# Kernel optimization log

Measured on AMD Instinct MI355X. Metric: run time of the kernel, lower is better.

The kernel has to match this reference:

```python
import jax, jax.numpy as jnp
import numpy as np

N_NODES = 50000
N_EDGES = 800000


def _gat_conv(x, src, dst, n, W, a_src, a_dst, b, concat):
    # x: [N, Fin]; W: [Fin, H*C]; a_src/a_dst: [H, C]; b: [H*C] or [C]
    H, C = a_src.shape
    h = (x @ W).reshape(n, H, C)                     # [N,H,C]
    alpha_src = jnp.sum(h * a_src[None], axis=-1)    # [N,H]
    alpha_dst = jnp.sum(h * a_dst[None], axis=-1)    # [N,H]
    e = alpha_src[src] + alpha_dst[dst]              # [E,H]
    e = jax.nn.leaky_relu(e, negative_slope=0.2)
    # segment softmax over incoming edges of each dst node
    m = jax.ops.segment_max(e, dst, num_segments=n)  # [N,H]
    ex = jnp.exp(e - m[dst])
    s = jax.ops.segment_sum(ex, dst, num_segments=n)
    alpha = ex / (s[dst] + 1e-16)                    # [E,H]
    msg = h[src] * alpha[:, :, None]                 # [E,H,C]
    out = jax.ops.segment_sum(msg, dst, num_segments=n)  # [N,H,C]
    out = out.reshape(n, H * C) if concat else out.mean(axis=1)
    return out + b


def setup_inputs() -> dict:
    key = jax.random.key(0)
    ks = jax.random.split(key, 12)
    d = {}
    d['x'] = jax.random.normal(ks[0], (N_NODES, 128), dtype=jnp.float32)
    d['edge_index'] = jax.random.randint(ks[1], (2, N_EDGES), 0, N_NODES, dtype=jnp.int32)
    s = 0.1
    d['w1'] = jax.random.normal(ks[2], (128, 128), dtype=jnp.float32) * s
    d['att_src1'] = jax.random.normal(ks[3], (2, 64), dtype=jnp.float32) * s
    d['att_dst1'] = jax.random.normal(ks[4], (2, 64), dtype=jnp.float32) * s
    d['b1'] = jnp.zeros((128,), jnp.float32)
    d['w2'] = jax.random.normal(ks[5], (128, 128), dtype=jnp.float32) * s
    d['att_src2'] = jax.random.normal(ks[6], (2, 64), dtype=jnp.float32) * s
    d['att_dst2'] = jax.random.normal(ks[7], (2, 64), dtype=jnp.float32) * s
    d['b2'] = jnp.zeros((128,), jnp.float32)
    d['w3'] = jax.random.normal(ks[8], (128, 40), dtype=jnp.float32) * s
    d['att_src3'] = jax.random.normal(ks[9], (1, 40), dtype=jnp.float32) * s
    d['att_dst3'] = jax.random.normal(ks[10], (1, 40), dtype=jnp.float32) * s
    d['b3'] = jnp.zeros((40,), jnp.float32)
    return d


def reference(x, edge_index, w1, att_src1, att_dst1, b1,
              w2, att_src2, att_dst2, b2, w3, att_src3, att_dst3, b3):
    n = x.shape[0]
    # PyG GATConv adds self-loops by default
    loop = jnp.arange(n, dtype=edge_index.dtype)
    src = jnp.concatenate([edge_index[0], loop])
    dst = jnp.concatenate([edge_index[1], loop])
    h = _gat_conv(x, src, dst, n, w1, att_src1, att_dst1, b1, concat=True)
    h = jax.nn.elu(h)  # dropout skipped (eval mode)
    h = _gat_conv(h, src, dst, n, w2, att_src2, att_dst2, b2, concat=True)
    h = jax.nn.elu(h)
    out = _gat_conv(h, src, dst, n, w3, att_src3, att_dst3, b3, concat=False)
    return out
```

## Files before the change

kernel.cpp:

```cpp
#include <hip/hip_runtime.h>
#include <hip/hip_fp16.h>

#define NN 50000
#define NE 800000
#define E2 850000
#define SCAN_NB 49
#define GEMM_BLKS 782
#define RANK_BLKS 3321

static inline int cdiv(long long a, int b) { return (int)((a + b - 1) / b); }

using half8  = __attribute__((ext_vector_type(8))) _Float16;
using floatx4 = __attribute__((ext_vector_type(4))) float;

struct __align__(16) h2x4 { __half2 a, b, c, d; };
struct __align__(8)  h2x2 { __half2 a, b; };

__device__ __forceinline__ void edge_sd(const int* __restrict__ ei, int e, int& s, int& d) {
    if (e < NE) { s = ei[e]; d = ei[NE + e]; }
    else { s = e - NE; d = s; }
}

__global__ __launch_bounds__(256) void prep_rank(const int* __restrict__ ei,
                                                 int* __restrict__ deg,
                                                 int* __restrict__ rank,
                                                 const float* __restrict__ x, __half* __restrict__ x16,
                                                 const float* __restrict__ w1, __half* __restrict__ wt1,
                                                 const float* __restrict__ w2, __half* __restrict__ wt2,
                                                 const float* __restrict__ w3, __half* __restrict__ wt3) {
    int b = blockIdx.x;
    if (b < RANK_BLKS) {
        int e = b * 256 + threadIdx.x;
        if (e < E2) {
            int d = (e < NE) ? ei[NE + e] : (e - NE);
            rank[e] = atomicAdd(&deg[d], 1);
        }
        return;
    }
    int tid = (b - RANK_BLKS) * 256 + threadIdx.x;
    int stride = (gridDim.x - RANK_BLKS) * 256;
    for (int i = tid; i < NN * 32; i += stride) {
        float4 v = *(const float4*)&x[(size_t)i * 4];
        h2x2 st;
        st.a = __floats2half2_rn(v.x, v.y);
        st.b = __floats2half2_rn(v.z, v.w);
        *(h2x2*)&x16[(size_t)i * 4] = st;
    }
    for (int i = tid; i < 128 * 128; i += stride)
        wt1[i] = __float2half(w1[(i & 127) * 128 + (i >> 7)]);
    for (int i = tid; i < 128 * 128; i += stride)
        wt2[i] = __float2half(w2[(i & 127) * 128 + (i >> 7)]);
    for (int i = tid; i < 40 * 128; i += stride)
        wt3[i] = __float2half(w3[(i & 127) * 40 + (i >> 7)]);
}

__global__ __launch_bounds__(256) void scan_all(const int* __restrict__ deg,
                                                int* __restrict__ rowp,
                                                int* __restrict__ bsums,
                                                int* __restrict__ ctr) {
    __shared__ int wsum[4];
    __shared__ int sh_pref[64];
    int tid = threadIdx.x;
    int base = blockIdx.x * 1024 + tid * 4;
    int4 v = make_int4(0, 0, 0, 0);
    if (base + 3 < NN) v = *(const int4*)&deg[base];
    else {
        if (base + 0 < NN) v.x = deg[base + 0];
        if (base + 1 < NN) v.y = deg[base + 1];
        if (base + 2 < NN) v.z = deg[base + 2];
    }
    v.y += v.x; v.z += v.y; v.w += v.z;
    int lane = tid & 63;
    int wid = tid >> 6;
    int t = v.w;
#pragma unroll
    for (int off = 1; off < 64; off <<= 1) {
        int u = __shfl_up(t, off, 64);
        if (lane >= off) t += u;
    }
    int excl = t - v.w;
    if (lane == 63) wsum[wid] = t;
    __syncthreads();
    int woff = 0;
    for (int w = 0; w < wid; ++w) woff += wsum[w];
    int add = excl + woff;
    if (tid == 255) {
        bsums[blockIdx.x] = add + v.w;
        __threadfence();
        atomicAdd(ctr, 1);
    }
    if (tid == 0) {
        while (__hip_atomic_load(ctr, __ATOMIC_ACQUIRE, __HIP_MEMORY_SCOPE_AGENT) < SCAN_NB) {
            __builtin_amdgcn_s_sleep(8);
        }
    }
    __syncthreads();
    if (tid < 64) {
        int bv = (tid < SCAN_NB)
            ? __hip_atomic_load(&bsums[tid], __ATOMIC_RELAXED, __HIP_MEMORY_SCOPE_AGENT) : 0;
        int s = bv;
#pragma unroll
        for (int off = 1; off < 64; off <<= 1) {
            int u = __shfl_up(s, off, 64);
            if (tid >= off) s += u;
        }
        sh_pref[tid] = s - bv;
    }
    __syncthreads();
    int boff = sh_pref[blockIdx.x];
    if (base == 0) rowp[0] = 0;
    if (base + 0 < NN) rowp[base + 1] = v.x + add + boff;
    if (base + 1 < NN) rowp[base + 2] = v.y + add + boff;
    if (base + 2 < NN) rowp[base + 3] = v.z + add + boff;
    if (base + 3 < NN) rowp[base + 4] = v.w + add + boff;
}

template<int MOUT, int H>
__device__ __forceinline__ void gemm_body(int bid, const __half* __restrict__ X,
                                          const __half* __restrict__ WT,
                                          const float* __restrict__ aS,
                                          const float* __restrict__ aD,
                                          __half* __restrict__ Ho,
                                          float* __restrict__ osrc,
                                          float* __restrict__ odst,
                                          __half* wlds) {
    constexpr int NT = (MOUT + 15) / 16;
    constexpr int NR = NT * 16;
    const int tid = threadIdx.x;
    for (int i = tid * 8; i < MOUT * 128; i += 2048) {
        half8 v = *(const half8*)&WT[i];
        *(half8*)&wlds[(i >> 7) * 136 + (i & 127)] = v;
    }
    if (NR > MOUT) {
        for (int i = tid * 8; i < (NR - MOUT) * 128; i += 2048) {
            half8 z = {};
            *(half8*)&wlds[(MOUT + (i >> 7)) * 136 + (i & 127)] = z;
        }
    }
    __syncthreads();

    const int lane = tid & 63;
    const int wid = tid >> 6;
    const int r0 = bid * 64 + wid * 16;
    const int arow = r0 + (lane & 15);
    const int lrow = (arow < NN) ? arow : (NN - 1);
    const int koff = (lane >> 4) * 8;
    const size_t xbase = (size_t)lrow * 128 + koff;
    half8 a0 = *(const half8*)&X[xbase];
    half8 a1 = *(const half8*)&X[xbase + 32];
    half8 a2 = *(const half8*)&X[xbase + 64];
    half8 a3 = *(const half8*)&X[xbase + 96];

    floatx4 acc[NT];
#pragma unroll
    for (int t = 0; t < NT; ++t) acc[t] = (floatx4){0.f, 0.f, 0.f, 0.f};

#pragma unroll
    for (int t = 0; t < NT; ++t) {
        const __half* wp = &wlds[(t * 16 + (lane & 15)) * 136 + koff];
        half8 b0 = *(const half8*)&wp[0];
        half8 b1 = *(const half8*)&wp[32];
        half8 b2 = *(const half8*)&wp[64];
        half8 b3 = *(const half8*)&wp[96];
        acc[t] = __builtin_amdgcn_mfma_f32_16x16x32_f16(a0, b0, acc[t], 0, 0, 0);
        acc[t] = __builtin_amdgcn_mfma_f32_16x16x32_f16(a1, b1, acc[t], 0, 0, 0);
        acc[t] = __builtin_amdgcn_mfma_f32_16x16x32_f16(a2, b2, acc[t], 0, 0, 0);
        acc[t] = __builtin_amdgcn_mfma_f32_16x16x32_f16(a3, b3, acc[t], 0, 0, 0);
    }

    const int cc = lane & 15;
    const int rbase = r0 + (lane >> 4) * 4;
    float ps[H][4], pd[H][4];
#pragma unroll
    for (int h = 0; h < H; ++h)
#pragma unroll
        for (int r = 0; r < 4; ++r) { ps[h][r] = 0.f; pd[h][r] = 0.f; }

#pragma unroll
    for (int t = 0; t < NT; ++t) {
        const int col = t * 16 + cc;
        const bool cv = (col < MOUT);
        const float as_ = cv ? aS[col] : 0.f;
        const float ad_ = cv ? aD[col] : 0.f;
        const int h = (H == 2) ? (t >> 2) : 0;
#pragma unroll
        for (int r = 0; r < 4; ++r) {
            ps[h][r] = fmaf(acc[t][r], as_, ps[h][r]);
            pd[h][r] = fmaf(acc[t][r], ad_, pd[h][r]);
        }
    }

    if constexpr (MOUT == 128) {
        __syncthreads();
        const int rowbase = wid * 16;
#pragma unroll
        for (int t = 0; t < NT; ++t)
#pragma unroll
            for (int r = 0; r < 4; ++r)
                wlds[(rowbase + (lane >> 4) * 4 + r) * 136 + t * 16 + cc] =
                    __float2half(acc[t][r]);
        __syncthreads();
#pragma unroll
        for (int p2 = 0; p2 < 4; ++p2) {
            int f = (p2 * 64 + lane) * 8;
            int row = f >> 7, col = f & 127;
            h2x4 v = *(h2x4*)&wlds[(rowbase + row) * 136 + col];
            int grow = r0 + row;
            if (grow < NN) *(h2x4*)&Ho[(size_t)grow * 128 + col] = v;
        }
    } else {
#pragma unroll
        for (int t = 0; t < NT; ++t) {
            const int col = t * 16 + cc;
            const bool cv = (col < MOUT);
#pragma unroll
            for (int r = 0; r < 4; ++r) {
                const int m = rbase + r;
                if (cv && m < NN) Ho[(size_t)m * MOUT + col] = __float2half(acc[t][r]);
            }
        }
    }

#pragma unroll
    for (int off = 1; off <= 8; off <<= 1) {
#pragma unroll
        for (int h = 0; h < H; ++h)
#pragma unroll
            for (int r = 0; r < 4; ++r) {
                ps[h][r] += __shfl_xor(ps[h][r], off, 64);
                pd[h][r] += __shfl_xor(pd[h][r], off, 64);
            }
    }
    if (cc == 0) {
#pragma unroll
        for (int r = 0; r < 4; ++r) {
            const int m = rbase + r;
            if (m < NN) {
#pragma unroll
                for (int h = 0; h < H; ++h) {
                    osrc[m * H + h] = ps[h][r];
                    odst[m * H + h] = pd[h][r];
                }
            }
        }
    }
}

__global__ __launch_bounds__(256) void gemm16_k128(const __half* __restrict__ X,
                                                   const __half* __restrict__ WT,
                                                   const float* __restrict__ aS,
                                                   const float* __restrict__ aD,
                                                   __half* __restrict__ Ho,
                                                   float* __restrict__ osrc,
                                                   float* __restrict__ odst) {
    __shared__ __half wlds[128 * 136];
    gemm_body<128, 2>(blockIdx.x, X, WT, aS, aD, Ho, osrc, odst, wlds);
}

__global__ __launch_bounds__(256) void gemm16_k40(const __half* __restrict__ X,
                                                  const __half* __restrict__ WT,
                                                  const float* __restrict__ aS,
                                                  const float* __restrict__ aD,
                                                  __half* __restrict__ Ho,
                                                  float* __restrict__ osrc,
                                                  float* __restrict__ odst) {
    __shared__ __half wlds[48 * 136];
    gemm_body<40, 1>(blockIdx.x, X, WT, aS, aD, Ho, osrc, odst, wlds);
}

__global__ __launch_bounds__(256) void gemm1_scat(const __half* __restrict__ X,
                                                  const __half* __restrict__ WT,
                                                  const float* __restrict__ aS,
                                                  const float* __restrict__ aD,
                                                  __half* __restrict__ Ho,
                                                  float* __restrict__ osrc,
                                                  float* __restrict__ odst,
                                                  const int* __restrict__ ei,
                                                  const int* __restrict__ rowp,
                                                  const int* __restrict__ rank,
                                                  int* __restrict__ csr_src) {
    __shared__ __half wlds[128 * 136];
    if (blockIdx.x < GEMM_BLKS) {
        gemm_body<128, 2>(blockIdx.x, X, WT, aS, aD, Ho, osrc, odst, wlds);
        return;
    }
    int e = (blockIdx.x - GEMM_BLKS) * 256 + threadIdx.x;
    if (e >= E2) return;
    int s, d; edge_sd(ei, e, s, d);
    csr_src[rowp[d] + rank[e]] = s;
}

__global__ __launch_bounds__(256) void agg_h2(const int* __restrict__ rowp,
                                              const int* __restrict__ csr_src,
                                              const __half* __restrict__ Hf,
                                              const float* __restrict__ osrc,
                                              const float* __restrict__ odst,
                                              const float* __restrict__ bias,
                                              __half* __restrict__ outp) {
    int n = blockIdx.x * 4 + (threadIdx.x >> 6);
    if (n >= NN) return;
    int lane = threadIdx.x & 63;
    int i0 = rowp[n], i1 = rowp[n + 1];
    int c = lane & 15;
    int slot = lane >> 4;
    int c8 = c * 8;
    int h2 = c >> 3;
    float adh = odst[n * 2 + h2];
    bool pl = ((c & 7) == 0);

    float4 lo0{0.f,0.f,0.f,0.f}, hi0{0.f,0.f,0.f,0.f};
    float4 lo1{0.f,0.f,0.f,0.f}, hi1{0.f,0.f,0.f,0.f};
    float psum = 0.f;

    int idx = i0 + slot;
    for (; idx + 12 < i1; idx += 16) {
        int s0 = csr_src[idx];
        int s1 = csr_src[idx + 4];
        int s2 = csr_src[idx + 8];
        int s3 = csr_src[idx + 12];
        float e0 = osrc[s0 * 2 + h2] + adh;
        float e1 = osrc[s1 * 2 + h2] + adh;
        float e2 = osrc[s2 * 2 + h2] + adh;
        float e3 = osrc[s3 * 2 + h2] + adh;
        e0 = (e0 >= 0.f) ? e0 : 0.2f * e0;
        e1 = (e1 >= 0.f) ? e1 : 0.2f * e1;
        e2 = (e2 >= 0.f) ? e2 : 0.2f * e2;
        e3 = (e3 >= 0.f) ? e3 : 0.2f * e3;
        float p0 = __expf(e0), p1 = __expf(e1), p2 = __expf(e2), p3 = __expf(e3);
        h2x4 hv0 = *(const h2x4*)&Hf[(size_t)s0 * 128 + c8];
        h2x4 hv1 = *(const h2x4*)&Hf[(size_t)s1 * 128 + c8];
        h2x4 hv2 = *(const h2x4*)&Hf[(size_t)s2 * 128 + c8];
        h2x4 hv3 = *(const h2x4*)&Hf[(size_t)s3 * 128 + c8];
        if (pl) psum += (p0 + p1) + (p2 + p3);
        float2 f;
        f = __half22float2(hv0.a); lo0.x = fmaf(f.x, p0, lo0.x); lo0.y = fmaf(f.y, p0, lo0.y);
        f = __half22float2(hv0.b); lo0.z = fmaf(f.x, p0, lo0.z); lo0.w = fmaf(f.y, p0, lo0.w);
        f = __half22float2(hv0.c); hi0.x = fmaf(f.x, p0, hi0.x); hi0.y = fmaf(f.y, p0, hi0.y);
        f = __half22float2(hv0.d); hi0.z = fmaf(f.x, p0, hi0.z); hi0.w = fmaf(f.y, p0, hi0.w);
        f = __half22float2(hv1.a); lo0.x = fmaf(f.x, p1, lo0.x); lo0.y = fmaf(f.y, p1, lo0.y);
        f = __half22float2(hv1.b); lo0.z = fmaf(f.x, p1, lo0.z); lo0.w = fmaf(f.y, p1, lo0.w);
        f = __half22float2(hv1.c); hi0.x = fmaf(f.x, p1, hi0.x); hi0.y = fmaf(f.y, p1, hi0.y);
        f = __half22float2(hv1.d); hi0.z = fmaf(f.x, p1, hi0.z); hi0.w = fmaf(f.y, p1, hi0.w);
        f = __half22float2(hv2.a); lo1.x = fmaf(f.x, p2, lo1.x); lo1.y = fmaf(f.y, p2, lo1.y);
        f = __half22float2(hv2.b); lo1.z = fmaf(f.x, p2, lo1.z); lo1.w = fmaf(f.y, p2, lo1.w);
        f = __half22float2(hv2.c); hi1.x = fmaf(f.x, p2, hi1.x); hi1.y = fmaf(f.y, p2, hi1.y);
        f = __half22float2(hv2.d); hi1.z = fmaf(f.x, p2, hi1.z); hi1.w = fmaf(f.y, p2, hi1.w);
        f = __half22float2(hv3.a); lo1.x = fmaf(f.x, p3, lo1.x); lo1.y = fmaf(f.y, p3, lo1.y);
        f = __half22float2(hv3.b); lo1.z = fmaf(f.x, p3, lo1.z); lo1.w = fmaf(f.y, p3, lo1.w);
        f = __half22float2(hv3.c); hi1.x = fmaf(f.x, p3, hi1.x); hi1.y = fmaf(f.y, p3, hi1.y);
        f = __half22float2(hv3.d); hi1.z = fmaf(f.x, p3, hi1.z); hi1.w = fmaf(f.y, p3, hi1.w);
    }
    {
        int id1 = idx + 4, id2 = idx + 8;
        bool v0 = idx < i1, v1 = id1 < i1, v2 = id2 < i1;
        int lim = i1 - 1;
        int s0 = csr_src[min(idx, lim)];
        int s1 = csr_src[min(id1, lim)];
        int s2 = csr_src[min(id2, lim)];
        float e0 = osrc[s0 * 2 + h2] + adh;
        float e1 = osrc[s1 * 2 + h2] + adh;
        float e2 = osrc[s2 * 2 + h2] + adh;
        e0 = (e0 >= 0.f) ? e0 : 0.2f * e0;
        e1 = (e1 >= 0.f) ? e1 : 0.2f * e1;
        e2 = (e2 >= 0.f) ? e2 : 0.2f * e2;
        float p0 = v0 ? __expf(e0) : 0.f;
        float p1 = v1 ? __expf(e1) : 0.f;
        float p2 = v2 ? __expf(e2) : 0.f;
        h2x4 hv0 = *(const h2x4*)&Hf[(size_t)s0 * 128 + c8];
        h2x4 hv1 = *(const h2x4*)&Hf[(size_t)s1 * 128 + c8];
        h2x4 hv2 = *(const h2x4*)&Hf[(size_t)s2 * 128 + c8];
        if (pl) psum += (p0 + p1) + p2;
        float2 f;
        f = __half22float2(hv0.a); lo0.x = fmaf(f.x, p0, lo0.x); lo0.y = fmaf(f.y, p0, lo0.y);
        f = __half22float2(hv0.b); lo0.z = fmaf(f.x, p0, lo0.z); lo0.w = fmaf(f.y, p0, lo0.w);
        f = __half22float2(hv0.c); hi0.x = fmaf(f.x, p0, hi0.x); hi0.y = fmaf(f.y, p0, hi0.y);
        f = __half22float2(hv0.d); hi0.z = fmaf(f.x, p0, hi0.z); hi0.w = fmaf(f.y, p0, hi0.w);
        f = __half22float2(hv1.a); lo0.x = fmaf(f.x, p1, lo0.x); lo0.y = fmaf(f.y, p1, lo0.y);
        f = __half22float2(hv1.b); lo0.z = fmaf(f.x, p1, lo0.z); lo0.w = fmaf(f.y, p1, lo0.w);
        f = __half22float2(hv1.c); hi0.x = fmaf(f.x, p1, hi0.x); hi0.y = fmaf(f.y, p1, hi0.y);
        f = __half22float2(hv1.d); hi0.z = fmaf(f.x, p1, hi0.z); hi0.w = fmaf(f.y, p1, hi0.w);
        f = __half22float2(hv2.a); lo1.x = fmaf(f.x, p2, lo1.x); lo1.y = fmaf(f.y, p2, lo1.y);
        f = __half22float2(hv2.b); lo1.z = fmaf(f.x, p2, lo1.z); lo1.w = fmaf(f.y, p2, lo1.w);
        f = __half22float2(hv2.c); hi1.x = fmaf(f.x, p2, hi1.x); hi1.y = fmaf(f.y, p2, hi1.y);
        f = __half22float2(hv2.d); hi1.z = fmaf(f.x, p2, hi1.z); hi1.w = fmaf(f.y, p2, hi1.w);
    }
    float4 lo{lo0.x + lo1.x, lo0.y + lo1.y, lo0.z + lo1.z, lo0.w + lo1.w};
    float4 hi{hi0.x + hi1.x, hi0.y + hi1.y, hi0.z + hi1.z, hi0.w + hi1.w};
#pragma unroll
    for (int off = 16; off <= 32; off <<= 1) {
        lo.x += __shfl_xor(lo.x, off, 64); lo.y += __shfl_xor(lo.y, off, 64);
        lo.z += __shfl_xor(lo.z, off, 64); lo.w += __shfl_xor(lo.w, off, 64);
        hi.x += __shfl_xor(hi.x, off, 64); hi.y += __shfl_xor(hi.y, off, 64);
        hi.z += __shfl_xor(hi.z, off, 64); hi.w += __shfl_xor(hi.w, off, 64);
        psum += __shfl_xor(psum, off, 64);
    }
    float sh = __shfl(psum, h2 * 8, 64);
    float inv = 1.f / (sh + 1e-16f);
    if (lane < 16) {
        float4 bl = *(const float4*)&bias[c8];
        float4 bh = *(const float4*)&bias[c8 + 4];
        float o0 = fmaf(lo.x, inv, bl.x), o1 = fmaf(lo.y, inv, bl.y);
        float o2 = fmaf(lo.z, inv, bl.z), o3 = fmaf(lo.w, inv, bl.w);
        float o4 = fmaf(hi.x, inv, bh.x), o5 = fmaf(hi.y, inv, bh.y);
        float o6 = fmaf(hi.z, inv, bh.z), o7 = fmaf(hi.w, inv, bh.w);
        o0 = (o0 > 0.f) ? o0 : (__expf(o0) - 1.f);
        o1 = (o1 > 0.f) ? o1 : (__expf(o1) - 1.f);
        o2 = (o2 > 0.f) ? o2 : (__expf(o2) - 1.f);
        o3 = (o3 > 0.f) ? o3 : (__expf(o3) - 1.f);
        o4 = (o4 > 0.f) ? o4 : (__expf(o4) - 1.f);
        o5 = (o5 > 0.f) ? o5 : (__expf(o5) - 1.f);
        o6 = (o6 > 0.f) ? o6 : (__expf(o6) - 1.f);
        o7 = (o7 > 0.f) ? o7 : (__expf(o7) - 1.f);
        h2x4 st;
        st.a = __floats2half2_rn(o0, o1);
        st.b = __floats2half2_rn(o2, o3);
        st.c = __floats2half2_rn(o4, o5);
        st.d = __floats2half2_rn(o6, o7);
        *(h2x4*)&outp[(size_t)n * 128 + c8] = st;
    }
}

__global__ __launch_bounds__(256) void agg_h1(const int* __restrict__ rowp,
                                              const int* __restrict__ csr_src,
                                              const __half* __restrict__ Hf,
                                              const float* __restrict__ osrc,
                                              const float* __restrict__ odst,
                                              const float* __restrict__ bias,
                                              float* __restrict__ outp) {
    int n = blockIdx.x * 4 + (threadIdx.x >> 6);
    if (n >= NN) return;
    int lane = threadIdx.x & 63;
    int i0 = rowp[n], i1 = rowp[n + 1];
    float ad = odst[n];
    int c = lane & 15;
    int slot = lane >> 4;
    bool cl = (c < 10);
    bool pl = (c == 0);
    float4 acc0{0.f,0.f,0.f,0.f}, acc1{0.f,0.f,0.f,0.f};
    float psum = 0.f;

    int idx = i0 + slot;
    for (; idx + 12 < i1; idx += 16) {
        int s0 = csr_src[idx];
        int s1 = csr_src[idx + 4];
        int s2 = csr_src[idx + 8];
        int s3 = csr_src[idx + 12];
        float e0 = osrc[s0] + ad, e1 = osrc[s1] + ad;
        float e2 = osrc[s2] + ad, e3 = osrc[s3] + ad;
        e0 = (e0 >= 0.f) ? e0 : 0.2f * e0;
        e1 = (e1 >= 0.f) ? e1 : 0.2f * e1;
        e2 = (e2 >= 0.f) ? e2 : 0.2f * e2;
        e3 = (e3 >= 0.f) ? e3 : 0.2f * e3;
        float p0 = __expf(e0), p1 = __expf(e1), p2 = __expf(e2), p3 = __expf(e3);
        if (pl) psum += (p0 + p1) + (p2 + p3);
        if (cl) {
            h2x2 hv0 = *(const h2x2*)&Hf[(size_t)s0 * 40 + c * 4];
            h2x2 hv1 = *(const h2x2*)&Hf[(size_t)s1 * 40 + c * 4];
            h2x2 hv2 = *(const h2x2*)&Hf[(size_t)s2 * 40 + c * 4];
            h2x2 hv3 = *(const h2x2*)&Hf[(size_t)s3 * 40 + c * 4];
            float2 f;
            f = __half22float2(hv0.a); acc0.x = fmaf(f.x, p0, acc0.x); acc0.y = fmaf(f.y, p0, acc0.y);
            f = __half22float2(hv0.b); acc0.z = fmaf(f.x, p0, acc0.z); acc0.w = fmaf(f.y, p0, acc0.w);
            f = __half22float2(hv1.a); acc1.x = fmaf(f.x, p1, acc1.x); acc1.y = fmaf(f.y, p1, acc1.y);
            f = __half22float2(hv1.b); acc1.z = fmaf(f.x, p1, acc1.z); acc1.w = fmaf(f.y, p1, acc1.w);
            f = __half22float2(hv2.a); acc0.x = fmaf(f.x, p2, acc0.x); acc0.y = fmaf(f.y, p2, acc0.y);
            f = __half22float2(hv2.b); acc0.z = fmaf(f.x, p2, acc0.z); acc0.w = fmaf(f.y, p2, acc0.w);
            f = __half22float2(hv3.a); acc1.x = fmaf(f.x, p3, acc1.x); acc1.y = fmaf(f.y, p3, acc1.y);
            f = __half22float2(hv3.b); acc1.z = fmaf(f.x, p3, acc1.z); acc1.w = fmaf(f.y, p3, acc1.w);
        }
    }
    {
        int id1 = idx + 4, id2 = idx + 8;
        bool v0 = idx < i1, v1 = id1 < i1, v2 = id2 < i1;
        int lim = i1 - 1;
        int s0 = csr_src[min(idx, lim)];
        int s1 = csr_src[min(id1, lim)];
        int s2 = csr_src[min(id2, lim)];
        float e0 = osrc[s0] + ad, e1 = osrc[s1] + ad, e2 = osrc[s2] + ad;
        e0 = (e0 >= 0.f) ? e0 : 0.2f * e0;
        e1 = (e1 >= 0.f) ? e1 : 0.2f * e1;
        e2 = (e2 >= 0.f) ? e2 : 0.2f * e2;
        float p0 = v0 ? __expf(e0) : 0.f;
        float p1 = v1 ? __expf(e1) : 0.f;
        float p2 = v2 ? __expf(e2) : 0.f;
        if (pl) psum += (p0 + p1) + p2;
        if (cl) {
            h2x2 hv0 = *(const h2x2*)&Hf[(size_t)s0 * 40 + c * 4];
            h2x2 hv1 = *(const h2x2*)&Hf[(size_t)s1 * 40 + c * 4];
            h2x2 hv2 = *(const h2x2*)&Hf[(size_t)s2 * 40 + c * 4];
            float2 f;
            f = __half22float2(hv0.a); acc0.x = fmaf(f.x, p0, acc0.x); acc0.y = fmaf(f.y, p0, acc0.y);
            f = __half22float2(hv0.b); acc0.z = fmaf(f.x, p0, acc0.z); acc0.w = fmaf(f.y, p0, acc0.w);
            f = __half22float2(hv1.a); acc1.x = fmaf(f.x, p1, acc1.x); acc1.y = fmaf(f.y, p1, acc1.y);
            f = __half22float2(hv1.b); acc1.z = fmaf(f.x, p1, acc1.z); acc1.w = fmaf(f.y, p1, acc1.w);
            f = __half22float2(hv2.a); acc0.x = fmaf(f.x, p2, acc0.x); acc0.y = fmaf(f.y, p2, acc0.y);
            f = __half22float2(hv2.b); acc0.z = fmaf(f.x, p2, acc0.z); acc0.w = fmaf(f.y, p2, acc0.w);
        }
    }
    float4 acc{acc0.x + acc1.x, acc0.y + acc1.y, acc0.z + acc1.z, acc0.w + acc1.w};
#pragma unroll
    for (int off = 16; off <= 32; off <<= 1) {
        acc.x += __shfl_xor(acc.x, off, 64);
        acc.y += __shfl_xor(acc.y, off, 64);
        acc.z += __shfl_xor(acc.z, off, 64);
        acc.w += __shfl_xor(acc.w, off, 64);
        psum += __shfl_xor(psum, off, 64);
    }
    float sh = __shfl(psum, 0, 64);
    float inv = 1.f / (sh + 1e-16f);
    if (lane < 10) {
        float4 b = *(const float4*)&bias[lane * 4];
        float4 o;
        o.x = fmaf(acc.x, inv, b.x);
        o.y = fmaf(acc.y, inv, b.y);
        o.z = fmaf(acc.z, inv, b.z);
        o.w = fmaf(acc.w, inv, b.w);
        *(float4*)&outp[(size_t)n * 40 + lane * 4] = o;
    }
}

extern "C" void kernel_launch(void* const* d_in, const int* in_sizes, int n_in,
                              void* d_out, int out_size, void* d_ws, size_t ws_size,
                              hipStream_t stream) {
    const float* x   = (const float*)d_in[0];
    const int*   ei  = (const int*)d_in[1];
    const float* w1  = (const float*)d_in[2];
    const float* as1 = (const float*)d_in[3];
    const float* ad1 = (const float*)d_in[4];
    const float* b1  = (const float*)d_in[5];
    const float* w2  = (const float*)d_in[6];
    const float* as2 = (const float*)d_in[7];
    const float* ad2 = (const float*)d_in[8];
    const float* b2  = (const float*)d_in[9];
    const float* w3  = (const float*)d_in[10];
    const float* as3 = (const float*)d_in[11];
    const float* ad3 = (const float*)d_in[12];
    const float* b3  = (const float*)d_in[13];
    float* out = (float*)d_out;

    char* p = (char*)d_ws;
    __half* x16   = (__half*)p; p += (size_t)NN * 128 * 2;
    __half* h16   = (__half*)p; p += (size_t)NN * 128 * 2;
    __half* f16   = (__half*)p; p += (size_t)NN * 128 * 2;
    __half* wt1   = (__half*)p; p += (size_t)128 * 128 * 2;
    __half* wt2   = (__half*)p; p += (size_t)128 * 128 * 2;
    __half* wt3   = (__half*)p; p += (size_t)64 * 128 * 2;
    float*  osrc  = (float*)p;  p += (size_t)NN * 2 * 4;
    float*  odst  = (float*)p;  p += (size_t)NN * 2 * 4;
    int*    rowp  = (int*)p;    p += (size_t)(NN + 1) * 4;
    int*    deg   = (int*)p;    p += (size_t)NN * 4;
    int*    ctr   = (int*)p;    p += (size_t)4;
    int*    rank  = (int*)p;    p += (size_t)E2 * 4;
    int*    bsums = (int*)p;    p += (size_t)64 * 4;
    int*    csrsrc= (int*)p;    p += (size_t)E2 * 4;

    const int edgeGrid = cdiv(E2, 256);
    const int nodeGrid = cdiv(NN, 4);

    hipMemsetAsync(deg, 0, (size_t)(NN + 1) * 4, stream);
    prep_rank<<<RANK_BLKS + 1024, 256, 0, stream>>>(ei, deg, rank, x, x16,
                                                    w1, wt1, w2, wt2, w3, wt3);
    scan_all<<<SCAN_NB, 256, 0, stream>>>(deg, rowp, bsums, ctr);

    gemm1_scat<<<GEMM_BLKS + edgeGrid, 256, 0, stream>>>(x16, wt1, as1, ad1, h16,
                                                         osrc, odst, ei, rowp, rank, csrsrc);
    agg_h2<<<nodeGrid, 256, 0, stream>>>(rowp, csrsrc, h16, osrc, odst, b1, f16);

    gemm16_k128<<<GEMM_BLKS, 256, 0, stream>>>(f16, wt2, as2, ad2, h16, osrc, odst);
    agg_h2<<<nodeGrid, 256, 0, stream>>>(rowp, csrsrc, h16, osrc, odst, b2, f16);

    gemm16_k40<<<GEMM_BLKS, 256, 0, stream>>>(f16, wt3, as3, ad3, h16, osrc, odst);
    agg_h1<<<nodeGrid, 256, 0, stream>>>(rowp, csrsrc, h16, osrc, odst, b3, out);
}
```

Before: 200.1 us.

## Replace global atomic degree counting with chunked LDS histograms and column scan

Builds the CSR by edge chunks. Each chunk counts in-degrees in a packed 16-bit shared-memory histogram, a column scan over chunks then yields per-chunk base offsets and the degrees. This replaces global atomics on the degree array and the separate memset. The fp32-to-fp16 conversion of x is folded into the first GEMM, which now loads fp32 directly, removing a full conversion pass and the x16 buffer. In exchange it adds two large count and base buffers of 128x25000 words, extra global traffic for them, and relies on per-chunk counts fitting in 16 bits.

```diff
diff --git a/kernel.cpp b/kernel.cpp
--- a/kernel.cpp
+++ b/kernel.cpp
@@ -6,7 +6,10 @@
 #define E2 850000
 #define SCAN_NB 49
 #define GEMM_BLKS 782
-#define RANK_BLKS 3321
+#define P_CH 128
+#define CH 6641
+#define HWORDS 12500
+#define COLS_BLKS 98
 
 static inline int cdiv(long long a, int b) { return (int)((a + b - 1) / b); }
 
@@ -21,31 +24,64 @@
     else { s = e - NE; d = s; }
 }
 
-__global__ __launch_bounds__(256) void prep_rank(const int* __restrict__ ei,
-                                                 int* __restrict__ deg,
-                                                 int* __restrict__ rank,
-                                                 const float* __restrict__ x, __half* __restrict__ x16,
-                                                 const float* __restrict__ w1, __half* __restrict__ wt1,
-                                                 const float* __restrict__ w2, __half* __restrict__ wt2,
-                                                 const float* __restrict__ w3, __half* __restrict__ wt3) {
+__device__ __forceinline__ half8 cvt_h8(float4 a, float4 b) {
+    half8 r;
+    r[0] = (_Float16)a.x; r[1] = (_Float16)a.y; r[2] = (_Float16)a.z; r[3] = (_Float16)a.w;
+    r[4] = (_Float16)b.x; r[5] = (_Float16)b.y; r[6] = (_Float16)b.z; r[7] = (_Float16)b.w;
+    return r;
+}
+
+__global__ __launch_bounds__(512) void hist_rank(const int* __restrict__ ei,
+                                                 unsigned* __restrict__ cnt,
+                                                 unsigned short* __restrict__ rank16) {
+    __shared__ unsigned hist[HWORDS];
+    const int c = blockIdx.x >> 1;
+    const int hf = blockIdx.x & 1;
+    const int tid = threadIdx.x;
+    for (int i = tid; i < HWORDS; i += 512) hist[i] = 0;
+    __syncthreads();
+    const int e0 = c * CH;
+    const int e1 = (e0 + CH < E2) ? e0 + CH : E2;
+    const int wlo = hf * HWORDS;
+    for (int e = e0 + tid; e < e1; e += 512) {
+        int d = (e < NE) ? ei[NE + e] : (e - NE);
+        int w = (d >> 1) - wlo;
+        if ((unsigned)w < HWORDS) {
+            unsigned sh = (d & 1) * 16;
+            unsigned old = atomicAdd(&hist[w], 1u << sh);
+            rank16[e] = (unsigned short)((old >> sh) & 0xffffu);
+        }
+    }
+    __syncthreads();
+    unsigned* dst = &cnt[(size_t)c * 25000 + wlo];
+    for (int i = tid; i < HWORDS; i += 512) dst[i] = hist[i];
+}
+
+__global__ __launch_bounds__(256) void colscan(const unsigned* __restrict__ cnt,
+                                               unsigned* __restrict__ chunkbase,
+                                               int* __restrict__ deg,
+                                               int* __restrict__ ctr,
+                                               const float* __restrict__ w1, __half* __restrict__ wt1,
+                                               const float* __restrict__ w2, __half* __restrict__ wt2,
+                                               const float* __restrict__ w3, __half* __restrict__ wt3) {
     int b = blockIdx.x;
-    if (b < RANK_BLKS) {
-        int e = b * 256 + threadIdx.x;
-        if (e < E2) {
-            int d = (e < NE) ? ei[NE + e] : (e - NE);
-            rank[e] = atomicAdd(&deg[d], 1);
-        }
+    if (b < COLS_BLKS) {
+        if (b == 0 && threadIdx.x == 0) *ctr = 0;
+        int w = b * 256 + threadIdx.x;
+        if (w >= 25000) return;
+        unsigned run = 0;
+#pragma unroll 4
+        for (int c = 0; c < P_CH; ++c) {
+            unsigned r = cnt[(size_t)c * 25000 + w];
+            chunkbase[(size_t)c * 25000 + w] = run;
+            run += r;
+        }
+        deg[2 * w]     = (int)(run & 0xffffu);
+        deg[2 * w + 1] = (int)(run >> 16);
         return;
     }
-    int tid = (b - RANK_BLKS) * 256 + threadIdx.x;
-    int stride = (gridDim.x - RANK_BLKS) * 256;
-    for (int i = tid; i < NN * 32; i += stride) {
-        float4 v = *(const float4*)&x[(size_t)i * 4];
-        h2x2 st;
-        st.a = __floats2half2_rn(v.x, v.y);
-        st.b = __floats2half2_rn(v.z, v.w);
-        *(h2x2*)&x16[(size_t)i * 4] = st;
-    }
+    int tid = (b - COLS_BLKS) * 256 + threadIdx.x;
+    int stride = (gridDim.x - COLS_BLKS) * 256;
     for (int i = tid; i < 128 * 128; i += stride)
         wt1[i] = __float2half(w1[(i & 127) * 128 + (i >> 7)]);
     for (int i = tid; i < 128 * 128; i += stride)
@@ -115,8 +151,8 @@
     if (base + 3 < NN) rowp[base + 4] = v.w + add + boff;
 }
 
-template<int MOUT, int H>
-__device__ __forceinline__ void gemm_body(int bid, const __half* __restrict__ X,
+template<int MOUT, int H, bool XF32>
+__device__ __forceinline__ void gemm_body(int bid, const void* __restrict__ Xv,
                                           const __half* __restrict__ WT,
                                           const float* __restrict__ aS,
                                           const float* __restrict__ aD,
@@ -145,11 +181,22 @@
     const int arow = r0 + (lane & 15);
     const int lrow = (arow < NN) ? arow : (NN - 1);
     const int koff = (lane >> 4) * 8;
-    const size_t xbase = (size_t)lrow * 128 + koff;
-    half8 a0 = *(const half8*)&X[xbase];
-    half8 a1 = *(const half8*)&X[xbase + 32];
-    half8 a2 = *(const half8*)&X[xbase + 64];
-    half8 a3 = *(const half8*)&X[xbase + 96];
+    half8 a0, a1, a2, a3;
+    if constexpr (XF32) {
+        const float* Xf = (const float*)Xv;
+        const size_t xb = (size_t)lrow * 128 + koff;
+        a0 = cvt_h8(*(const float4*)&Xf[xb +  0], *(const float4*)&Xf[xb +  4]);
+        a1 = cvt_h8(*(const float4*)&Xf[xb + 32], *(const float4*)&Xf[xb + 36]);
+        a2 = cvt_h8(*(const float4*)&Xf[xb + 64], *(const float4*)&Xf[xb + 68]);
+        a3 = cvt_h8(*(const float4*)&Xf[xb + 96], *(const float4*)&Xf[xb + 100]);
+    } else {
+        const __half* Xh = (const __half*)Xv;
+        const size_t xb = (size_t)lrow * 128 + koff;
+        a0 = *(const half8*)&Xh[xb];
+        a1 = *(const half8*)&Xh[xb + 32];
+        a2 = *(const half8*)&Xh[xb + 64];
+        a3 = *(const half8*)&Xh[xb + 96];
+    }
 
     floatx4 acc[NT];
 #pragma unroll
@@ -254,7 +301,7 @@
                                                    float* __restrict__ osrc,
                                                    float* __restrict__ odst) {
     __shared__ __half wlds[128 * 136];
-    gemm_body<128, 2>(blockIdx.x, X, WT, aS, aD, Ho, osrc, odst, wlds);
+    gemm_body<128, 2, false>(blockIdx.x, X, WT, aS, aD, Ho, osrc, odst, wlds);
 }
 
 __global__ __launch_bounds__(256) void gemm16_k40(const __half* __restrict__ X,
@@ -265,10 +312,10 @@
                                                   float* __restrict__ osrc,
                                                   float* __restrict__ odst) {
     __shared__ __half wlds[48 * 136];
-    gemm_body<40, 1>(blockIdx.x, X, WT, aS, aD, Ho, osrc, odst, wlds);
-}
-
-__global__ __launch_bounds__(256) void gemm1_scat(const __half* __restrict__ X,
+    gemm_body<40, 1, false>(blockIdx.x, X, WT, aS, aD, Ho, osrc, odst, wlds);
+}
+
+__global__ __launch_bounds__(256) void gemm1_scat(const float* __restrict__ X,
                                                   const __half* __restrict__ WT,
                                                   const float* __restrict__ aS,
                                                   const float* __restrict__ aD,
@@ -277,17 +324,21 @@
                                                   float* __restrict__ odst,
                                                   const int* __restrict__ ei,
                                                   const int* __restrict__ rowp,
-                                                  const int* __restrict__ rank,
+                                                  const unsigned short* __restrict__ rank16,
+                                                  const unsigned* __restrict__ chunkbase,
                                                   int* __restrict__ csr_src) {
     __shared__ __half wlds[128 * 136];
     if (blockIdx.x < GEMM_BLKS) {
-        gemm_body<128, 2>(blockIdx.x, X, WT, aS, aD, Ho, osrc, odst, wlds);
+        gemm_body<128, 2, true>(blockIdx.x, X, WT, aS, aD, Ho, osrc, odst, wlds);
         return;
     }
     int e = (blockIdx.x - GEMM_BLKS) * 256 + threadIdx.x;
     if (e >= E2) return;
+    int c = e / CH;
     int s, d; edge_sd(ei, e, s, d);
-    csr_src[rowp[d] + rank[e]] = s;
+    unsigned cb = chunkbase[(size_t)c * 25000 + (d >> 1)];
+    int off = (int)((cb >> ((d & 1) * 16)) & 0xffffu);
+    csr_src[rowp[d] + off + (int)rank16[e]] = s;
 }
 
 __global__ __launch_bounds__(256) void agg_h2(const int* __restrict__ rowp,
@@ -539,31 +590,33 @@
     float* out = (float*)d_out;
 
     char* p = (char*)d_ws;
-    __half* x16   = (__half*)p; p += (size_t)NN * 128 * 2;
-    __half* h16   = (__half*)p; p += (size_t)NN * 128 * 2;
-    __half* f16   = (__half*)p; p += (size_t)NN * 128 * 2;
-    __half* wt1   = (__half*)p; p += (size_t)128 * 128 * 2;
-    __half* wt2   = (__half*)p; p += (size_t)128 * 128 * 2;
-    __half* wt3   = (__half*)p; p += (size_t)64 * 128 * 2;
-    float*  osrc  = (float*)p;  p += (size_t)NN * 2 * 4;
-    float*  odst  = (float*)p;  p += (size_t)NN * 2 * 4;
-    int*    rowp  = (int*)p;    p += (size_t)(NN + 1) * 4;
-    int*    deg   = (int*)p;    p += (size_t)NN * 4;
-    int*    ctr   = (int*)p;    p += (size_t)4;
-    int*    rank  = (int*)p;    p += (size_t)E2 * 4;
-    int*    bsums = (int*)p;    p += (size_t)64 * 4;
-    int*    csrsrc= (int*)p;    p += (size_t)E2 * 4;
+    __half*   h16    = (__half*)p;   p += (size_t)NN * 128 * 2;
+    __half*   f16    = (__half*)p;   p += (size_t)NN * 128 * 2;
+    unsigned* cnt    = (unsigned*)p; p += (size_t)P_CH * 25000 * 4;
+    unsigned* cbase  = (unsigned*)p; p += (size_t)P_CH * 25000 * 4;
+    __half*   wt1    = (__half*)p;   p += (size_t)128 * 128 * 2;
+    __half*   wt2    = (__half*)p;   p += (size_t)128 * 128 * 2;
+    __half*   wt3    = (__half*)p;   p += (size_t)64 * 128 * 2;
+    float*    osrc   = (float*)p;    p += (size_t)NN * 2 * 4;
+    float*    odst   = (float*)p;    p += (size_t)NN * 2 * 4;
+    int*      rowp   = (int*)p;      p += (size_t)(NN + 4) * 4;
+    int*      deg    = (int*)p;      p += (size_t)NN * 4;
+    unsigned short* rank16 = (unsigned short*)p; p += (size_t)E2 * 2;
+    int*      bsums  = (int*)p;      p += (size_t)64 * 4;
+    int*      ctr    = (int*)p;      p += (size_t)4 * 4;
+    int*      csrsrc = (int*)p;      p += (size_t)E2 * 4;
 
     const int edgeGrid = cdiv(E2, 256);
     const int nodeGrid = cdiv(NN, 4);
 
-    hipMemsetAsync(deg, 0, (size_t)(NN + 1) * 4, stream);
-    prep_rank<<<RANK_BLKS + 1024, 256, 0, stream>>>(ei, deg, rank, x, x16,
-                                                    w1, wt1, w2, wt2, w3, wt3);
+    hist_rank<<<P_CH * 2, 512, 0, stream>>>(ei, cnt, rank16);
+    colscan<<<COLS_BLKS + 64, 256, 0, stream>>>(cnt, cbase, deg, ctr,
+                                                w1, wt1, w2, wt2, w3, wt3);
     scan_all<<<SCAN_NB, 256, 0, stream>>>(deg, rowp, bsums, ctr);
 
-    gemm1_scat<<<GEMM_BLKS + edgeGrid, 256, 0, stream>>>(x16, wt1, as1, ad1, h16,
-                                                         osrc, odst, ei, rowp, rank, csrsrc);
+    gemm1_scat<<<GEMM_BLKS + edgeGrid, 256, 0, stream>>>(x, wt1, as1, ad1, h16,
+                                                         osrc, odst, ei, rowp,
+                                                         rank16, cbase, csrsrc);
     agg_h2<<<nodeGrid, 256, 0, stream>>>(rowp, csrsrc, h16, osrc, odst, b1, f16);
 
     gemm16_k128<<<GEMM_BLKS, 256, 0, stream>>>(f16, wt2, as2, ad2, h16, osrc, odst);
```

After: 183.7 us. 1.09x faster.
